# Optimization experiments

Measured on AMD Instinct MI355X. Metric: run time of the kernel, lower is better.

The kernel has to match this reference:

```python
import jax, jax.numpy as jnp
import numpy as np

N_NODES = 100000
N_EDGES = 600000
FEAT = 128
HID = 128
N_LAYERS = 5
BN_EPS = 1e-5


def setup_inputs() -> dict:
    key = jax.random.key(0)
    ks = jax.random.split(key, 10)
    x = jax.random.normal(ks[0], (N_NODES, FEAT), dtype=jnp.float32)
    edge_index = jax.random.randint(ks[1], (2, N_EDGES), 0, N_NODES, dtype=jnp.int64)
    # conv weights: all layers are 128->128 (glorot-ish scale)
    conv_w = jax.random.normal(ks[2], (N_LAYERS, HID, HID), dtype=jnp.float32) * (1.0 / np.sqrt(HID))
    conv_b = jnp.zeros((N_LAYERS, HID), dtype=jnp.float32)
    bn_gamma = jnp.ones((N_LAYERS, HID), dtype=jnp.float32)
    bn_beta = jnp.zeros((N_LAYERS, HID), dtype=jnp.float32)
    fc_w = jax.random.normal(ks[3], (1, HID), dtype=jnp.float32) * (1.0 / np.sqrt(HID))
    fc_b = jnp.zeros((1,), dtype=jnp.float32)
    return {"x": x, "edge_index": edge_index, "conv_w": conv_w, "conv_b": conv_b,
            "bn_gamma": bn_gamma, "bn_beta": bn_beta, "fc_w": fc_w, "fc_b": fc_b}


def _gcn_norm(edge_index, n_nodes):
    # PyG gcn_norm with add_self_loops=True, edge_weight=None (ones)
    row = jnp.concatenate([edge_index[0], jnp.arange(n_nodes, dtype=edge_index.dtype)])
    col = jnp.concatenate([edge_index[1], jnp.arange(n_nodes, dtype=edge_index.dtype)])
    ew = jnp.ones(row.shape[0], dtype=jnp.float32)
    deg = jax.ops.segment_sum(ew, col, num_segments=n_nodes)
    dinv = jnp.where(deg > 0, jax.lax.rsqrt(deg), 0.0)
    norm = dinv[row] * ew * dinv[col]  # [E + N]
    return row, col, norm


def reference(x, edge_index, conv_w, conv_b, bn_gamma, bn_beta, fc_w, fc_b):
    n = x.shape[0]
    row, col, norm = _gcn_norm(edge_index, n)
    for l in range(N_LAYERS):
        h = x @ conv_w[l]                                   # [N, H]
        msg = norm[:, None] * h[row]                        # gather + scale
        h = jax.ops.segment_sum(msg, col, num_segments=n)   # scatter-add
        h = h + conv_b[l]
        # BatchNorm1d (training-mode batch stats, biased var)
        mean = jnp.mean(h, axis=0)
        var = jnp.var(h, axis=0)
        h = bn_gamma[l] * (h - mean) * jax.lax.rsqrt(var + BN_EPS) + bn_beta[l]
        x = jax.nn.relu(h)
    edge_emb = x[edge_index[0]] * x[edge_index[1]]          # [E, H]
    out = edge_emb @ fc_w.T + fc_b                          # [E, 1]
    return jax.nn.sigmoid(out)
```

## Files before the change

### kernel.cpp

```cpp
#include <hip/hip_runtime.h>

#define NN 100000
#define NE 600000
#define HH 128
#define NL 5
#define BN_EPS 1e-5f
#define NB 391
#define NBS 782
#define L2B 32
#define RPB 25

typedef float f4 __attribute__((ext_vector_type(4)));
typedef float f2 __attribute__((ext_vector_type(2)));
typedef _Float16 h8 __attribute__((ext_vector_type(8)));
typedef _Float16 h2x __attribute__((ext_vector_type(2)));

__global__ void k_probe(const unsigned long long* __restrict__ e, int* __restrict__ flag) {
    if (blockIdx.x == 0 && threadIdx.x == 0) {
        int ok = 1;
        for (int i = 0; i < 64; ++i)
            if (e[i] >= (unsigned long long)NN) ok = 0;
        *flag = ok;
    }
}

__global__ void k_convert(const void* __restrict__ src, const int* __restrict__ flag,
                          int* __restrict__ dst) {
    int i = blockIdx.x * 256 + threadIdx.x;
    if (i >= 2 * NE) return;
    if (*flag) dst[i] = (int)((const long long*)src)[i];
    else       dst[i] = ((const int*)src)[i];
}

__global__ void k_zero(int* __restrict__ p, int n) {
    int i = blockIdx.x * 256 + threadIdx.x;
    if (i < n) p[i] = 0;
}

__global__ void k_count_deg(const int* __restrict__ col, int* __restrict__ degi) {
    int e = blockIdx.x * 256 + threadIdx.x;
    if (e < NE) atomicAdd(&degi[col[e]], 1);
}

__global__ void k_dinv(const int* __restrict__ degi, float* __restrict__ dinv) {
    int i = blockIdx.x * 256 + threadIdx.x;
    if (i < NN) dinv[i] = rsqrtf((float)degi[i] + 1.0f);
}

__global__ __launch_bounds__(256) void k_scan1(const int* __restrict__ degi,
                                               int* __restrict__ incl,
                                               int* __restrict__ blocksums) {
    __shared__ int sd[256];
    int tid = threadIdx.x;
    int i = blockIdx.x * 256 + tid;
    int v = (i < NN) ? degi[i] : 0;
    sd[tid] = v;
    __syncthreads();
#pragma unroll
    for (int off = 1; off < 256; off <<= 1) {
        int t = (tid >= off) ? sd[tid - off] : 0;
        __syncthreads();
        sd[tid] += t;
        __syncthreads();
    }
    if (i < NN) incl[i] = sd[tid];
    if (tid == 255) blocksums[blockIdx.x] = sd[255];
}

__global__ __launch_bounds__(512) void k_scan2(const int* __restrict__ blocksums,
                                               int* __restrict__ blockoffs) {
    __shared__ int sd[512];
    int tid = threadIdx.x;
    int v = (tid < NB) ? blocksums[tid] : 0;
    sd[tid] = v;
    __syncthreads();
#pragma unroll
    for (int off = 1; off < 512; off <<= 1) {
        int t = (tid >= off) ? sd[tid - off] : 0;
        __syncthreads();
        sd[tid] += t;
        __syncthreads();
    }
    if (tid < NB) blockoffs[tid] = sd[tid] - v;
}

__global__ void k_scan3(const int* __restrict__ incl, const int* __restrict__ degi,
                        const int* __restrict__ blockoffs,
                        int* __restrict__ offsets, int* __restrict__ cursor) {
    int i = blockIdx.x * 256 + threadIdx.x;
    if (i >= NN) return;
    offsets[i] = incl[i] - degi[i] + blockoffs[blockIdx.x];
    cursor[i] = 0;
}

__global__ void k_scatter(const int* __restrict__ ei, const float* __restrict__ dinv,
                          const int* __restrict__ offsets, int* __restrict__ cursor,
                          int2* __restrict__ csr) {
    int e = blockIdx.x * 256 + threadIdx.x;
    if (e >= NE) return;
    int r = ei[e], c = ei[NE + e];
    int pos = offsets[c] + atomicAdd(&cursor[c], 1);
    int2 v;
    v.x = r;
    v.y = __float_as_int(dinv[r] * dinv[c]);
    csr[pos] = v;
}

__global__ void k_wt(const float* __restrict__ W, _Float16* __restrict__ Wt_hi,
                     _Float16* __restrict__ Wt_lo) {
    int gid = blockIdx.x * 256 + threadIdx.x;
    if (gid >= NL * HH * HH) return;
    int l = gid >> 14;
    int rem = gid & 16383;
    int n = rem >> 7;
    int k = rem & 127;
    float w = W[l * HH * HH + k * HH + n];
    _Float16 hi = (_Float16)w;
    _Float16 lo = (_Float16)(w - (float)hi);
    Wt_hi[gid] = hi;
    Wt_lo[gid] = lo;
}

__global__ __launch_bounds__(256) void k_gemm(const float* __restrict__ A,
                                              const _Float16* __restrict__ Wt_hi,
                                              const _Float16* __restrict__ Wt_lo,
                                              const float* __restrict__ stats,
                                              const float* __restrict__ gamma,
                                              const float* __restrict__ beta,
                                              int mode, float negmul,
                                              float* __restrict__ C) {
    __shared__ float s_sc[128], s_sh[128];
    const int tid  = threadIdx.x;
    if (tid < 128) {
        float sc = 1.0f, sh = 0.0f;
        if (mode) {
            const float inv_n = 1.0f / (float)NN;
            float mean = stats[tid] * inv_n;
            float var  = stats[128 + tid] * inv_n - mean * mean;
            sc = gamma[tid] * rsqrtf(var + BN_EPS);
            sh = beta[tid] - mean * sc;
        }
        s_sc[tid] = sc;
        s_sh[tid] = sh;
    }
    __syncthreads();

    const int wave = tid >> 6;
    const int lane = tid & 63;
    const int r    = lane & 15;
    const int kg   = lane >> 4;
    const int row0 = blockIdx.x * 128 + wave * 32;

    f4 acc[2][8];
#pragma unroll
    for (int m = 0; m < 2; ++m)
#pragma unroll
        for (int n = 0; n < 8; ++n) acc[m][n] = (f4)0.0f;

    int ra0 = row0 + r;       if (ra0 >= NN) ra0 = NN - 1;
    int ra1 = row0 + 16 + r;  if (ra1 >= NN) ra1 = NN - 1;
    const float* A0 = A + (size_t)ra0 * HH + kg * 8;
    const float* A1 = A + (size_t)ra1 * HH + kg * 8;
    const _Float16* BpH = Wt_hi + (size_t)r * HH + kg * 8;
    const _Float16* BpL = Wt_lo + (size_t)r * HH + kg * 8;

#pragma unroll
    for (int kc = 0; kc < 4; ++kc) {
        const int k0 = kc * 32 + kg * 8;
        f4 scA = *reinterpret_cast<const f4*>(&s_sc[k0]);
        f4 scB = *reinterpret_cast<const f4*>(&s_sc[k0 + 4]);
        f4 shA = *reinterpret_cast<const f4*>(&s_sh[k0]);
        f4 shB = *reinterpret_cast<const f4*>(&s_sh[k0 + 4]);
        f4 a0x = *reinterpret_cast<const f4*>(A0 + kc * 32);
        f4 a0y = *reinterpret_cast<const f4*>(A0 + kc * 32 + 4);
        f4 a1x = *reinterpret_cast<const f4*>(A1 + kc * 32);
        f4 a1y = *reinterpret_cast<const f4*>(A1 + kc * 32 + 4);
        h8 a0hi, a0lo, a1hi, a1lo;
#pragma unroll
        for (int j = 0; j < 4; ++j) {
            float t;
            t = fmaf(a0x[j], scA[j], shA[j]); t = fmaxf(t, t * negmul);
            a0hi[j] = (_Float16)t;      a0lo[j] = (_Float16)(t - (float)a0hi[j]);
            t = fmaf(a0y[j], scB[j], shB[j]); t = fmaxf(t, t * negmul);
            a0hi[j + 4] = (_Float16)t;  a0lo[j + 4] = (_Float16)(t - (float)a0hi[j + 4]);
            t = fmaf(a1x[j], scA[j], shA[j]); t = fmaxf(t, t * negmul);
            a1hi[j] = (_Float16)t;      a1lo[j] = (_Float16)(t - (float)a1hi[j]);
            t = fmaf(a1y[j], scB[j], shB[j]); t = fmaxf(t, t * negmul);
            a1hi[j + 4] = (_Float16)t;  a1lo[j + 4] = (_Float16)(t - (float)a1hi[j + 4]);
        }
#pragma unroll
        for (int n = 0; n < 8; ++n) {
            h8 bh = *reinterpret_cast<const h8*>(BpH + (size_t)n * 16 * HH + kc * 32);
            h8 bl = *reinterpret_cast<const h8*>(BpL + (size_t)n * 16 * HH + kc * 32);
            acc[0][n] = __builtin_amdgcn_mfma_f32_16x16x32_f16(bh, a0hi, acc[0][n], 0, 0, 0);
            acc[0][n] = __builtin_amdgcn_mfma_f32_16x16x32_f16(bl, a0hi, acc[0][n], 0, 0, 0);
            acc[0][n] = __builtin_amdgcn_mfma_f32_16x16x32_f16(bh, a0lo, acc[0][n], 0, 0, 0);
            acc[1][n] = __builtin_amdgcn_mfma_f32_16x16x32_f16(bh, a1hi, acc[1][n], 0, 0, 0);
            acc[1][n] = __builtin_amdgcn_mfma_f32_16x16x32_f16(bl, a1hi, acc[1][n], 0, 0, 0);
            acc[1][n] = __builtin_amdgcn_mfma_f32_16x16x32_f16(bh, a1lo, acc[1][n], 0, 0, 0);
        }
    }

#pragma unroll
    for (int m = 0; m < 2; ++m) {
        int rr = row0 + m * 16 + r;
        if (rr < NN) {
            float* Crow = C + (size_t)rr * HH + kg * 4;
#pragma unroll
            for (int n = 0; n < 8; ++n)
                *reinterpret_cast<f4*>(Crow + n * 16) = acc[m][n];
        }
    }
}

__global__ __launch_bounds__(256) void k_gather(const float* __restrict__ h1,
                                                const int* __restrict__ offsets,
                                                const int* __restrict__ degi,
                                                const int2* __restrict__ csr,
                                                const float* __restrict__ dinv,
                                                float* __restrict__ h2) {
    int gid  = blockIdx.x * 256 + threadIdx.x;
    int node = gid >> 6;
    int lane = gid & 63;
    if (node >= NN) return;
    float di = dinv[node];
    f2 acc0 = reinterpret_cast<const f2*>(h1 + (size_t)node * HH)[lane] * (di * di);
    f2 acc1 = (f2)0.0f, acc2 = (f2)0.0f, acc3 = (f2)0.0f;
    const int start = offsets[node];
    const int end   = start + degi[node];
    for (int b = start; b < end; b += 4) {
        int2 ce0 = csr[b];
        int2 ce1 = (b + 1 < end) ? csr[b + 1] : make_int2(0, 0);
        int2 ce2 = (b + 2 < end) ? csr[b + 2] : make_int2(0, 0);
        int2 ce3 = (b + 3 < end) ? csr[b + 3] : make_int2(0, 0);
        f2 v0 = reinterpret_cast<const f2*>(h1 + (size_t)ce0.x * HH)[lane];
        f2 v1 = reinterpret_cast<const f2*>(h1 + (size_t)ce1.x * HH)[lane];
        f2 v2 = reinterpret_cast<const f2*>(h1 + (size_t)ce2.x * HH)[lane];
        f2 v3 = reinterpret_cast<const f2*>(h1 + (size_t)ce3.x * HH)[lane];
        acc0 += v0 * __int_as_float(ce0.y);
        acc1 += v1 * __int_as_float(ce1.y);
        acc2 += v2 * __int_as_float(ce2.y);
        acc3 += v3 * __int_as_float(ce3.y);
    }
    acc0 += acc2;
    acc1 += acc3;
    acc0 += acc1;
    reinterpret_cast<f2*>(h2 + (size_t)node * HH)[lane] = acc0;
}

__global__ __launch_bounds__(256) void k_bnstats(const float* __restrict__ h,
                                                 float* __restrict__ partial) {
    __shared__ f4 ls[8][32];
    __shared__ f4 lss[8][32];
    const int q  = threadIdx.x & 31;
    const int rg = threadIdx.x >> 5;
    const int r0 = blockIdx.x * 128;
    int rend = r0 + 128;
    if (rend > NN) rend = NN;
    f4 s = (f4)0.0f, ss = (f4)0.0f;
    for (int r = r0 + rg; r < rend; r += 8) {
        f4 v = *reinterpret_cast<const f4*>(h + (size_t)r * HH + q * 4);
        s += v;
        ss += v * v;
    }
    ls[rg][q] = s;
    lss[rg][q] = ss;
    __syncthreads();
    if (rg == 0) {
        f4 st = ls[0][q];
#pragma unroll
        for (int g = 1; g < 8; ++g) st += ls[g][q];
        *reinterpret_cast<f4*>(&partial[(size_t)blockIdx.x * 256 + q * 4]) = st;
    } else if (rg == 1) {
        f4 sq = lss[0][q];
#pragma unroll
        for (int g = 1; g < 8; ++g) sq += lss[g][q];
        *reinterpret_cast<f4*>(&partial[(size_t)blockIdx.x * 256 + 128 + q * 4]) = sq;
    }
}

__global__ void k_sred1(const float* __restrict__ partial, float* __restrict__ level2) {
    int c = threadIdx.x;
    int b0 = blockIdx.x * RPB;
    int b1 = b0 + RPB;
    if (b1 > NBS) b1 = NBS;
    float s = 0.0f;
    for (int b = b0; b < b1; ++b) s += partial[(size_t)b * 256 + c];
    level2[(size_t)blockIdx.x * 256 + c] = s;
}

__global__ void k_sred2(const float* __restrict__ level2, float* __restrict__ stats) {
    int c = threadIdx.x;
    float s = 0.0f;
#pragma unroll
    for (int b = 0; b < L2B; ++b) s += level2[(size_t)b * 256 + c];
    stats[c] = s;
}

__global__ void k_bnapply(const float* __restrict__ h2, const float* __restrict__ stats,
                          const float* __restrict__ gamma, const float* __restrict__ beta,
                          _Float16* __restrict__ xh) {
    int idx = blockIdx.x * 256 + threadIdx.x;
    if (idx >= NN * 64) return;
    int cp = idx & 63;
    int c0 = 2 * cp, c1 = c0 + 1;
    const float inv_n = 1.0f / (float)NN;
    float m0 = stats[c0] * inv_n, m1 = stats[c1] * inv_n;
    float v0s = stats[128 + c0] * inv_n - m0 * m0;
    float v1s = stats[128 + c1] * inv_n - m1 * m1;
    float sc0 = gamma[c0] * rsqrtf(v0s + BN_EPS);
    float sc1 = gamma[c1] * rsqrtf(v1s + BN_EPS);
    float sh0 = beta[c0] - m0 * sc0;
    float sh1 = beta[c1] - m1 * sc1;
    f2 v = reinterpret_cast<const f2*>(h2)[idx];
    float t0 = fmaf(v[0], sc0, sh0);
    float t1 = fmaf(v[1], sc1, sh1);
    t0 = fmaxf(t0, 0.0f);
    t1 = fmaxf(t1, 0.0f);
    h2x o;
    o[0] = (_Float16)t0;
    o[1] = (_Float16)t1;
    reinterpret_cast<h2x*>(xh)[idx] = o;
}

__global__ __launch_bounds__(256) void k_final(const _Float16* __restrict__ x,
                                               const int* __restrict__ ei,
                                               const float* __restrict__ fcw,
                                               const float* __restrict__ fcb,
                                               float* __restrict__ out) {
    int gid  = blockIdx.x * 256 + threadIdx.x;
    int e    = gid >> 4;
    int l16  = gid & 15;
    if (e >= NE) return;
    int a = ei[e];
    int b = ei[NE + e];
    h8 va = *reinterpret_cast<const h8*>(x + (size_t)a * HH + l16 * 8);
    h8 vb = *reinterpret_cast<const h8*>(x + (size_t)b * HH + l16 * 8);
    f4 w0 = *reinterpret_cast<const f4*>(fcw + l16 * 8);
    f4 w1 = *reinterpret_cast<const f4*>(fcw + l16 * 8 + 4);
    float p = 0.0f;
#pragma unroll
    for (int j = 0; j < 4; ++j) {
        p += (float)va[j] * (float)vb[j] * w0[j];
        p += (float)va[j + 4] * (float)vb[j + 4] * w1[j];
    }
#pragma unroll
    for (int off = 8; off > 0; off >>= 1) p += __shfl_xor(p, off, 64);
    if (l16 == 0) out[e] = 1.0f / (1.0f + expf(-(p + fcb[0])));
}

extern "C" void kernel_launch(void* const* d_in, const int* in_sizes, int n_in,
                              void* d_out, int out_size, void* d_ws, size_t ws_size,
                              hipStream_t stream) {
    const float* x   = (const float*)d_in[0];
    const void*  ei_raw = d_in[1];
    const float* cw  = (const float*)d_in[2];
    const float* gam = (const float*)d_in[4];
    const float* bet = (const float*)d_in[5];
    const float* fcw = (const float*)d_in[6];
    const float* fcb = (const float*)d_in[7];
    float* out = (float*)d_out;

    const size_t NH = (size_t)NN * HH;
    unsigned char* p = (unsigned char*)d_ws;
    float* h1 = (float*)p;       p += NH * 4;
    float* h2 = (float*)p;       p += NH * 4;
    _Float16* xh = (_Float16*)p; p += NH * 2;
    _Float16* WtH = (_Float16*)p; p += (size_t)NL * HH * HH * 2;
    _Float16* WtL = (_Float16*)p; p += (size_t)NL * HH * HH * 2;
    int2*  csr   = (int2*)p;     p += (size_t)NE * 8;
    float* dinv  = (float*)p;    p += NN * 4;
    float* stats = (float*)p;    p += NL * 256 * 4;
    float* partial = (float*)p;  p += (size_t)NBS * 256 * 4;
    float* level2  = (float*)p;  p += (size_t)L2B * 256 * 4;
    int*   ei    = (int*)p;      p += (size_t)2 * NE * 4;
    int*   degi  = (int*)p;      p += NN * 4;
    int*   incl  = (int*)p;      p += NN * 4;
    int*   offsets = (int*)p;    p += NN * 4;
    int*   cursor  = (int*)p;    p += NN * 4;
    int*   blocksums = (int*)p;  p += NB * 4;
    int*   blockoffs = (int*)p;  p += NB * 4;
    int*   flag  = (int*)p;

    k_probe<<<1, 64, 0, stream>>>((const unsigned long long*)ei_raw, flag);
    k_convert<<<(2 * NE + 255) / 256, 256, 0, stream>>>(ei_raw, flag, ei);

    k_zero<<<(NN + 255) / 256, 256, 0, stream>>>(degi, NN);
    k_count_deg<<<(NE + 255) / 256, 256, 0, stream>>>(ei + NE, degi);
    k_dinv<<<(NN + 255) / 256, 256, 0, stream>>>(degi, dinv);
    k_scan1<<<NB, 256, 0, stream>>>(degi, incl, blocksums);
    k_scan2<<<1, 512, 0, stream>>>(blocksums, blockoffs);
    k_scan3<<<NB, 256, 0, stream>>>(incl, degi, blockoffs, offsets, cursor);
    k_scatter<<<(NE + 255) / 256, 256, 0, stream>>>(ei, dinv, offsets, cursor, csr);

    k_wt<<<(NL * HH * HH + 255) / 256, 256, 0, stream>>>(cw, WtH, WtL);

    for (int l = 0; l < NL; ++l) {
        k_gemm<<<(NN + 127) / 128, 256, 0, stream>>>(
            (l == 0) ? x : h2, WtH + (size_t)l * HH * HH, WtL + (size_t)l * HH * HH,
            (l == 0) ? stats : stats + (size_t)(l - 1) * 256,
            (l == 0) ? gam : gam + (size_t)(l - 1) * HH,
            (l == 0) ? bet : bet + (size_t)(l - 1) * HH,
            (l == 0) ? 0 : 1, (l == 0) ? 1.0f : 0.0f, h1);
        k_gather<<<(NN * 64 + 255) / 256, 256, 0, stream>>>(h1, offsets, degi, csr, dinv, h2);
        k_bnstats<<<NBS, 256, 0, stream>>>(h2, partial);
        k_sred1<<<L2B, 256, 0, stream>>>(partial, level2);
        k_sred2<<<1, 256, 0, stream>>>(level2, stats + (size_t)l * 256);
    }
    k_bnapply<<<(NN * 64 + 255) / 256, 256, 0, stream>>>(h2, stats + (size_t)(NL - 1) * 256,
                                                         gam + (size_t)(NL - 1) * HH,
                                                         bet + (size_t)(NL - 1) * HH, xh);
    k_final<<<(NE * 16 + 255) / 256, 256, 0, stream>>>(xh, ei, fcw, fcb, out);
}
```

Baseline: 776.7 us.

## Stage weights in LDS for GEMM, precompute BN scale/shift, widen gather unroll

The GEMM now copies the hi/lo fp16 weight tiles (64 KB total) into shared memory in MFMA fragment order, so each wave reads B operands from LDS instead of global memory. Computing the BN scale and shift moves into a separate tiny kernel per layer, and the GEMM reads the results directly from global memory. The gather kernel unrolls its edge loop to 8 independent loads and accumulators to raise memory-level parallelism. The tradeoffs are 64 KB of LDS per block, which limits occupancy, one extra launch per layer, and more registers in the gather.

New measurement: 733.4 us. -5.6%, faster.

```diff
diff --git a/kernel.cpp b/kernel.cpp
--- a/kernel.cpp
+++ b/kernel.cpp
@@ -121,27 +121,41 @@
     Wt_lo[gid] = lo;
 }
 
+__global__ void k_prep(const float* __restrict__ stats, const float* __restrict__ gamma,
+                       const float* __restrict__ beta, int mode, float* __restrict__ scsh) {
+    int k = threadIdx.x;
+    float sc = 1.0f, sh = 0.0f;
+    if (mode) {
+        const float inv_n = 1.0f / (float)NN;
+        float mean = stats[k] * inv_n;
+        float var  = stats[128 + k] * inv_n - mean * mean;
+        sc = gamma[k] * rsqrtf(var + BN_EPS);
+        sh = beta[k] - mean * sc;
+    }
+    scsh[k] = sc;
+    scsh[128 + k] = sh;
+}
+
 __global__ __launch_bounds__(256) void k_gemm(const float* __restrict__ A,
                                               const _Float16* __restrict__ Wt_hi,
                                               const _Float16* __restrict__ Wt_lo,
-                                              const float* __restrict__ stats,
-                                              const float* __restrict__ gamma,
-                                              const float* __restrict__ beta,
-                                              int mode, float negmul,
+                                              const float* __restrict__ scsh,
+                                              float negmul,
                                               float* __restrict__ C) {
-    __shared__ float s_sc[128], s_sh[128];
-    const int tid  = threadIdx.x;
-    if (tid < 128) {
-        float sc = 1.0f, sh = 0.0f;
-        if (mode) {
-            const float inv_n = 1.0f / (float)NN;
-            float mean = stats[tid] * inv_n;
-            float var  = stats[128 + tid] * inv_n - mean * mean;
-            sc = gamma[tid] * rsqrtf(var + BN_EPS);
-            sh = beta[tid] - mean * sc;
-        }
-        s_sc[tid] = sc;
-        s_sh[tid] = sh;
+    __shared__ _Float16 sBH[16384];
+    __shared__ _Float16 sBL[16384];
+    const int tid = threadIdx.x;
+
+#pragma unroll
+    for (int it = 0; it < 8; ++it) {
+        int g  = it * 256 + tid;
+        int r  = g & 15;
+        int kg = (g >> 4) & 3;
+        int kc = (g >> 6) & 3;
+        int n  = g >> 8;
+        int glob = (n * 16 + r) * HH + kc * 32 + kg * 8;
+        *reinterpret_cast<h8*>(&sBH[g * 8]) = *reinterpret_cast<const h8*>(Wt_hi + glob);
+        *reinterpret_cast<h8*>(&sBL[g * 8]) = *reinterpret_cast<const h8*>(Wt_lo + glob);
     }
     __syncthreads();
 
@@ -161,16 +175,14 @@
     int ra1 = row0 + 16 + r;  if (ra1 >= NN) ra1 = NN - 1;
     const float* A0 = A + (size_t)ra0 * HH + kg * 8;
     const float* A1 = A + (size_t)ra1 * HH + kg * 8;
-    const _Float16* BpH = Wt_hi + (size_t)r * HH + kg * 8;
-    const _Float16* BpL = Wt_lo + (size_t)r * HH + kg * 8;
 
 #pragma unroll
     for (int kc = 0; kc < 4; ++kc) {
         const int k0 = kc * 32 + kg * 8;
-        f4 scA = *reinterpret_cast<const f4*>(&s_sc[k0]);
-        f4 scB = *reinterpret_cast<const f4*>(&s_sc[k0 + 4]);
-        f4 shA = *reinterpret_cast<const f4*>(&s_sh[k0]);
-        f4 shB = *reinterpret_cast<const f4*>(&s_sh[k0 + 4]);
+        f4 scA = *reinterpret_cast<const f4*>(scsh + k0);
+        f4 scB = *reinterpret_cast<const f4*>(scsh + k0 + 4);
+        f4 shA = *reinterpret_cast<const f4*>(scsh + 128 + k0);
+        f4 shB = *reinterpret_cast<const f4*>(scsh + 128 + k0 + 4);
         f4 a0x = *reinterpret_cast<const f4*>(A0 + kc * 32);
         f4 a0y = *reinterpret_cast<const f4*>(A0 + kc * 32 + 4);
         f4 a1x = *reinterpret_cast<const f4*>(A1 + kc * 32);
@@ -190,8 +202,9 @@
         }
 #pragma unroll
         for (int n = 0; n < 8; ++n) {
-            h8 bh = *reinterpret_cast<const h8*>(BpH + (size_t)n * 16 * HH + kc * 32);
-            h8 bl = *reinterpret_cast<const h8*>(BpL + (size_t)n * 16 * HH + kc * 32);
+            int g = n * 256 + kc * 64 + lane;
+            h8 bh = *reinterpret_cast<const h8*>(&sBH[g * 8]);
+            h8 bl = *reinterpret_cast<const h8*>(&sBL[g * 8]);
             acc[0][n] = __builtin_amdgcn_mfma_f32_16x16x32_f16(bh, a0hi, acc[0][n], 0, 0, 0);
             acc[0][n] = __builtin_amdgcn_mfma_f32_16x16x32_f16(bl, a0hi, acc[0][n], 0, 0, 0);
             acc[0][n] = __builtin_amdgcn_mfma_f32_16x16x32_f16(bh, a0lo, acc[0][n], 0, 0, 0);
@@ -224,28 +237,32 @@
     int lane = gid & 63;
     if (node >= NN) return;
     float di = dinv[node];
-    f2 acc0 = reinterpret_cast<const f2*>(h1 + (size_t)node * HH)[lane] * (di * di);
-    f2 acc1 = (f2)0.0f, acc2 = (f2)0.0f, acc3 = (f2)0.0f;
+    f2 acc[8];
+    acc[0] = reinterpret_cast<const f2*>(h1 + (size_t)node * HH)[lane] * (di * di);
+#pragma unroll
+    for (int j = 1; j < 8; ++j) acc[j] = (f2)0.0f;
     const int start = offsets[node];
     const int end   = start + degi[node];
-    for (int b = start; b < end; b += 4) {
-        int2 ce0 = csr[b];
-        int2 ce1 = (b + 1 < end) ? csr[b + 1] : make_int2(0, 0);
-        int2 ce2 = (b + 2 < end) ? csr[b + 2] : make_int2(0, 0);
-        int2 ce3 = (b + 3 < end) ? csr[b + 3] : make_int2(0, 0);
-        f2 v0 = reinterpret_cast<const f2*>(h1 + (size_t)ce0.x * HH)[lane];
-        f2 v1 = reinterpret_cast<const f2*>(h1 + (size_t)ce1.x * HH)[lane];
-        f2 v2 = reinterpret_cast<const f2*>(h1 + (size_t)ce2.x * HH)[lane];
-        f2 v3 = reinterpret_cast<const f2*>(h1 + (size_t)ce3.x * HH)[lane];
-        acc0 += v0 * __int_as_float(ce0.y);
-        acc1 += v1 * __int_as_float(ce1.y);
-        acc2 += v2 * __int_as_float(ce2.y);
-        acc3 += v3 * __int_as_float(ce3.y);
-    }
-    acc0 += acc2;
-    acc1 += acc3;
-    acc0 += acc1;
-    reinterpret_cast<f2*>(h2 + (size_t)node * HH)[lane] = acc0;
+    for (int b = start; b < end; b += 8) {
+        int2 ce[8];
+        ce[0] = csr[b];
+#pragma unroll
+        for (int j = 1; j < 8; ++j)
+            ce[j] = (b + j < end) ? csr[b + j] : make_int2(0, 0);
+        f2 v[8];
+#pragma unroll
+        for (int j = 0; j < 8; ++j)
+            v[j] = reinterpret_cast<const f2*>(h1 + (size_t)ce[j].x * HH)[lane];
+#pragma unroll
+        for (int j = 0; j < 8; ++j)
+            acc[j] += v[j] * __int_as_float(ce[j].y);
+    }
+#pragma unroll
+    for (int j = 0; j < 4; ++j) acc[j] += acc[j + 4];
+    acc[0] += acc[2];
+    acc[1] += acc[3];
+    acc[0] += acc[1];
+    reinterpret_cast<f2*>(h2 + (size_t)node * HH)[lane] = acc[0];
 }
 
 __global__ __launch_bounds__(256) void k_bnstats(const float* __restrict__ h,
@@ -371,6 +388,7 @@
     int2*  csr   = (int2*)p;     p += (size_t)NE * 8;
     float* dinv  = (float*)p;    p += NN * 4;
     float* stats = (float*)p;    p += NL * 256 * 4;
+    float* scsh  = (float*)p;    p += NL * 256 * 4;
     float* partial = (float*)p;  p += (size_t)NBS * 256 * 4;
     float* level2  = (float*)p;  p += (size_t)L2B * 256 * 4;
     int*   ei    = (int*)p;      p += (size_t)2 * NE * 4;
@@ -396,12 +414,14 @@
     k_wt<<<(NL * HH * HH + 255) / 256, 256, 0, stream>>>(cw, WtH, WtL);
 
     for (int l = 0; l < NL; ++l) {
-        k_gemm<<<(NN + 127) / 128, 256, 0, stream>>>(
-            (l == 0) ? x : h2, WtH + (size_t)l * HH * HH, WtL + (size_t)l * HH * HH,
+        k_prep<<<1, 128, 0, stream>>>(
             (l == 0) ? stats : stats + (size_t)(l - 1) * 256,
             (l == 0) ? gam : gam + (size_t)(l - 1) * HH,
             (l == 0) ? bet : bet + (size_t)(l - 1) * HH,
-            (l == 0) ? 0 : 1, (l == 0) ? 1.0f : 0.0f, h1);
+            (l == 0) ? 0 : 1, scsh + (size_t)l * 256);
+        k_gemm<<<(NN + 127) / 128, 256, 0, stream>>>(
+            (l == 0) ? x : h2, WtH + (size_t)l * HH * HH, WtL + (size_t)l * HH * HH,
+            scsh + (size_t)l * 256, (l == 0) ? 1.0f : 0.0f, h1);
         k_gather<<<(NN * 64 + 255) / 256, 256, 0, stream>>>(h1, offsets, degi, csr, dinv, h2);
         k_bnstats<<<NBS, 256, 0, stream>>>(h2, partial);
         k_sred1<<<L2B, 256, 0, stream>>>(partial, level2);
```
